# Kernel optimization log

Hardware: AMD Instinct MI355X
Metric: run time of the kernel (lower is better)

## Reference

```python
import jax, jax.numpy as jnp
import numpy as np

HEAD_NUM = 4
B, S, D = 8, 1024, 512


def setup_inputs() -> dict:
    k = jax.random.key(0)
    kq, kk, kv = jax.random.split(k, 3)
    return {
        "query": jax.random.normal(kq, (B, S, D), dtype=jnp.float32),
        "key": jax.random.normal(kk, (B, S, D), dtype=jnp.float32),
        "value": jax.random.normal(kv, (B, S, D), dtype=jnp.float32),
    }


def _corr_attention(q, k, v):
    # q,k,v: [B, H, S, hd]
    score = jnp.einsum('bhqd,bhkd->bhqk', q, k)  # raw dot products
    len_q = jnp.sqrt(jnp.sum(q * q, axis=-1))    # [B,H,S]
    len_k = jnp.sqrt(jnp.sum(k * k, axis=-1))    # [B,H,S]
    score = score / (len_q[..., :, None] * len_k[..., None, :])  # cosine similarity
    signal = jnp.sign(score)
    flat = jnp.abs(score).reshape(-1)            # global flatten across B,H,S,S
    n = flat.shape[0]
    idx = jnp.argsort(-flat)                     # descending sort indices
    prob = (jnp.arange(n, dtype=flat.dtype) + 1.0) / n  # (1/n, 2/n, ..., 1)
    ranked = flat.at[idx].set(prob)              # rank-transform: largest -> smallest prob
    score = (-jnp.log(ranked)).reshape(signal.shape) * signal
    return jnp.einsum('bhqk,bhkd->bhqd', score, v)


def reference(query, key, value):
    b, s, d = query.shape
    h = HEAD_NUM
    q = query.reshape(b, s, h, -1).transpose(0, 2, 1, 3)
    k = key.reshape(b, s, h, -1).transpose(0, 2, 1, 3)
    v = value.reshape(b, s, h, -1).transpose(0, 2, 1, 3)
    out = _corr_attention(q, k, v)               # [B,H,S,hd]
    return out.transpose(0, 2, 1, 3).reshape(b, s, d)
```

## Files before the change

kernel.cpp:

```cpp
#include <hip/hip_runtime.h>
#include <math.h>

#define BB 8
#define SS 1024
#define DD 512
#define HH 4
#define HD 128
#define N_SC (BB*HH*SS*SS)

#define NB 8192
#define BINA 20971.52f
#define NPART 512

#define OFF_S     0
#define SZ_S      ((size_t)N_SC*2)
#define OFF_QN    (OFF_S + SZ_S)
#define SZ_QN     ((size_t)BB*SS*DD*2)
#define OFF_KN    (OFF_QN + SZ_QN)
#define OFF_VT    (OFF_KN + SZ_QN)
#define OFF_PARTS (OFF_VT + SZ_QN)
#define SZ_PARTS  ((size_t)NPART*NB*2)
#define OFF_HIST  (OFF_PARTS + SZ_PARTS)

typedef __bf16 bf16x8 __attribute__((ext_vector_type(8)));
typedef float  f32x4  __attribute__((ext_vector_type(4)));
typedef unsigned short ushort_t;

__device__ __forceinline__ unsigned bf16rne(float x) {
  unsigned b = __float_as_uint(x);
  return (b + 0x7FFFu + ((b >> 16) & 1u)) >> 16;
}

__global__ __launch_bounds__(256) void prep_kernel(
    const float* __restrict__ q, const float* __restrict__ k,
    unsigned* __restrict__ qn, unsigned* __restrict__ kn) {
  int t = threadIdx.x, lane = t & 63;
  int row = blockIdx.x*4 + (t >> 6);
  const float* src; unsigned* dst; int r;
  if (row < 32768) { src = q; dst = qn; r = row; }
  else             { src = k; dst = kn; r = row - 32768; }
  int b = r >> 12, s = (r >> 2) & 1023, h = r & 3;
  float2 v = *(const float2*)(src + ((size_t)(b*1024 + s))*512 + h*128 + lane*2);
  float sum = v.x*v.x + v.y*v.y;
  #pragma unroll
  for (int off = 32; off; off >>= 1) sum += __shfl_xor(sum, off, 64);
  float inv = rsqrtf(sum);
  unsigned u = bf16rne(v.x*inv) | (bf16rne(v.y*inv) << 16);
  dst[(size_t)((b*4 + h)*1024 + s)*64 + lane] = u;
}

__global__ __launch_bounds__(256) void vt_kernel(
    const float* __restrict__ v, unsigned* __restrict__ vt) {
  __shared__ float T[64][65];
  int t = threadIdx.x;
  int s0 = blockIdx.x*64, d0 = blockIdx.y*64, bh = blockIdx.z;
  int b = bh >> 2, h = bh & 3;
  #pragma unroll
  for (int i = 0; i < 16; i++) {
    int idx = t + i*256, rs = idx >> 6, cd = idx & 63;
    T[rs][cd] = v[((size_t)(b*1024 + s0 + rs))*512 + h*128 + d0 + cd];
  }
  __syncthreads();
  #pragma unroll
  for (int i = 0; i < 8; i++) {
    int idx = t + i*256, rd = idx >> 5, c2 = (idx & 31)*2;
    unsigned u = bf16rne(T[c2][rd]) | (bf16rne(T[c2+1][rd]) << 16);
    vt[(size_t)(bh*128 + d0 + rd)*512 + (s0 + c2)/2] = u;
  }
}

__global__ __launch_bounds__(256) void scores_kernel(
    const ushort_t* __restrict__ qn, const ushort_t* __restrict__ kn,
    ushort_t* __restrict__ S) {
  __shared__ ushort_t Qs[128*128];
  __shared__ ushort_t Ks[128*128];
  int t = threadIdx.x;
  int bh = blockIdx.z, sq0 = blockIdx.y*128, sk0 = blockIdx.x*128;

  const uint4* qg = (const uint4*)qn + (size_t)(bh*1024 + sq0)*16;
  const uint4* kg = (const uint4*)kn + (size_t)(bh*1024 + sk0)*16;
  #pragma unroll
  for (int i = 0; i < 8; i++) {
    int idx = t + i*256, row = idx >> 4, g = idx & 15;
    int sw = g ^ (row & 15);
    *(uint4*)&Qs[row*128 + sw*8] = qg[row*16 + g];
    *(uint4*)&Ks[row*128 + sw*8] = kg[row*16 + g];
  }
  __syncthreads();

  int w = t >> 6, lane = t & 63, m16 = lane & 15, q2 = lane >> 4;
  int wm = (w >> 1)*64, wn = (w & 1)*64;
  f32x4 acc[4][4];
  #pragma unroll
  for (int i = 0; i < 4; i++)
    #pragma unroll
    for (int j = 0; j < 4; j++) acc[i][j] = (f32x4){0.f,0.f,0.f,0.f};

  #pragma unroll
  for (int ks = 0; ks < 4; ks++) {
    int sw = ((ks*4 + q2) ^ m16)*8;
    bf16x8 a[4], bb[4];
    #pragma unroll
    for (int i = 0; i < 4; i++) a[i]  = *(const bf16x8*)&Qs[(wm + i*16 + m16)*128 + sw];
    #pragma unroll
    for (int j = 0; j < 4; j++) bb[j] = *(const bf16x8*)&Ks[(wn + j*16 + m16)*128 + sw];
    #pragma unroll
    for (int i = 0; i < 4; i++)
      #pragma unroll
      for (int j = 0; j < 4; j++)
        acc[i][j] = __builtin_amdgcn_mfma_f32_16x16x32_bf16(a[i], bb[j], acc[i][j], 0, 0, 0);
  }

  size_t Sbase = (size_t)bh << 20;
  #pragma unroll
  for (int i = 0; i < 4; i++)
    #pragma unroll
    for (int p = 0; p < 4; p++) {
      int row = sq0 + wm + i*16 + q2*4 + p;
      #pragma unroll
      for (int j = 0; j < 4; j++) {
        int col = sk0 + wn + j*16 + m16;
        S[Sbase + ((size_t)row << 10) + col] = (ushort_t)bf16rne(acc[i][j][p]);
      }
    }
}

__global__ __launch_bounds__(1024) void hist_kernel(
    const ushort_t* __restrict__ S, ushort_t* __restrict__ parts) {
  __shared__ unsigned h[NB];
  int t = threadIdx.x;
  #pragma unroll
  for (int i = t; i < NB; i += 1024) h[i] = 0;
  __syncthreads();
  const uint4* p = (const uint4*)S;
  size_t base = (size_t)blockIdx.x * 8192;
  #pragma unroll
  for (int it = 0; it < 8; it++) {
    uint4 v = p[base + t + it*1024];
    unsigned ws[4] = {v.x, v.y, v.z, v.w};
    #pragma unroll
    for (int j = 0; j < 4; j++) {
      float flo = __uint_as_float(ws[j] << 16);
      float fhi = __uint_as_float(ws[j] & 0xFFFF0000u);
      atomicAdd(&h[(unsigned)fminf(flo*flo*BINA, 8191.0f)], 1u);
      atomicAdd(&h[(unsigned)fminf(fhi*fhi*BINA, 8191.0f)], 1u);
    }
  }
  __syncthreads();
  ushort_t* dst = parts + (size_t)blockIdx.x*NB;
  for (int i = t; i < NB; i += 1024) dst[i] = (ushort_t)min(h[i], 65535u);
}

__global__ __launch_bounds__(256) void reduce_kernel(
    const ushort_t* __restrict__ parts, unsigned* __restrict__ hist) {
  int bin = blockIdx.x*256 + threadIdx.x;
  unsigned s = 0;
  #pragma unroll 8
  for (int p = 0; p < NPART; p++) s += parts[(size_t)p*NB + bin];
  hist[bin] = s;
}

__global__ __launch_bounds__(1024) void scan_kernel(unsigned* hist) {
  __shared__ unsigned d[1024];
  int t = threadIdx.x;
  unsigned loc[8];
  uint4 a = ((const uint4*)hist)[t*2], b2 = ((const uint4*)hist)[t*2+1];
  loc[0]=a.x; loc[1]=a.y; loc[2]=a.z; loc[3]=a.w;
  loc[4]=b2.x; loc[5]=b2.y; loc[6]=b2.z; loc[7]=b2.w;
  unsigned tot = 0;
  #pragma unroll
  for (int j = 0; j < 8; j++) tot += loc[j];
  d[t] = tot; __syncthreads();
  for (int off = 1; off < 1024; off <<= 1) {
    unsigned x = (t >= off) ? d[t - off] : 0u;
    __syncthreads();
    d[t] += x;
    __syncthreads();
  }
  unsigned run = d[t] - tot;
  const float inv_n = 1.0f / (float)N_SC;
  float* w = (float*)hist;
  #pragma unroll
  for (int j = 0; j < 8; j++) {
    run += loc[j];
    float rm = (float)(N_SC - run) + 0.5f*(float)(loc[j] + 1u);
    w[t*8 + j] = -logf(rm * inv_n);
  }
}

__global__ __launch_bounds__(256) void out_kernel(
    const ushort_t* __restrict__ S, const float* __restrict__ wmag,
    const ushort_t* __restrict__ vt, float* __restrict__ out) {
  __shared__ ushort_t Ws[64*128];
  __shared__ ushort_t Vs[128*128];
  __shared__ float    Wl[NB];
  int t = threadIdx.x;
  int bh = blockIdx.y, q0 = blockIdx.x*64;
  int b = bh >> 2, h = bh & 3;

  #pragma unroll
  for (int i = 0; i < 8; i++) {
    int idx = t + i*256;
    ((uint4*)Wl)[idx] = ((const uint4*)wmag)[idx];
  }

  int w = t >> 6, lane = t & 63, m16 = lane & 15, q2 = lane >> 4;
  int wq = (w >> 1)*32, wd = (w & 1)*64;
  f32x4 acc[2][4];
  #pragma unroll
  for (int i = 0; i < 2; i++)
    #pragma unroll
    for (int j = 0; j < 4; j++) acc[i][j] = (f32x4){0.f,0.f,0.f,0.f};

  for (int kc = 0; kc < 8; kc++) {
    __syncthreads();
    #pragma unroll
    for (int i = 0; i < 4; i++) {
      int idx = t + i*256, row = idx >> 4, g = idx & 15;
      uint4 sv = ((const uint4*)S)[(size_t)(bh*1024 + q0 + row)*128 + kc*16 + g];
      unsigned wsrc[4] = {sv.x, sv.y, sv.z, sv.w};
      unsigned wdst[4];
      #pragma unroll
      for (int j = 0; j < 4; j++) {
        float flo = __uint_as_float(wsrc[j] << 16);
        float fhi = __uint_as_float(wsrc[j] & 0xFFFF0000u);
        float mlo = Wl[(unsigned)fminf(flo*flo*BINA, 8191.0f)];
        float mhi = Wl[(unsigned)fminf(fhi*fhi*BINA, 8191.0f)];
        float wlo = (flo == 0.f) ? 0.f : copysignf(mlo, flo);
        float whi = (fhi == 0.f) ? 0.f : copysignf(mhi, fhi);
        wdst[j] = bf16rne(wlo) | (bf16rne(whi) << 16);
      }
      uint4 wv = {wdst[0], wdst[1], wdst[2], wdst[3]};
      *(uint4*)&Ws[row*128 + ((g ^ (row & 15))*8)] = wv;
    }
    #pragma unroll
    for (int i = 0; i < 8; i++) {
      int idx = t + i*256, row = idx >> 4, g = idx & 15;
      uint4 vv = ((const uint4*)vt)[(size_t)(bh*128 + row)*128 + kc*16 + g];
      *(uint4*)&Vs[row*128 + ((g ^ (row & 15))*8)] = vv;
    }
    __syncthreads();
    #pragma unroll
    for (int ks = 0; ks < 4; ks++) {
      int sw = ((ks*4 + q2) ^ m16)*8;
      bf16x8 a[2], bb[4];
      #pragma unroll
      for (int i = 0; i < 2; i++) a[i]  = *(const bf16x8*)&Ws[(wq + i*16 + m16)*128 + sw];
      #pragma unroll
      for (int j = 0; j < 4; j++) bb[j] = *(const bf16x8*)&Vs[(wd + j*16 + m16)*128 + sw];
      #pragma unroll
      for (int i = 0; i < 2; i++)
        #pragma unroll
        for (int j = 0; j < 4; j++)
          acc[i][j] = __builtin_amdgcn_mfma_f32_16x16x32_bf16(a[i], bb[j], acc[i][j], 0, 0, 0);
    }
  }

  #pragma unroll
  for (int i = 0; i < 2; i++)
    #pragma unroll
    for (int p = 0; p < 4; p++) {
      int qrow = q0 + wq + i*16 + q2*4 + p;
      #pragma unroll
      for (int j = 0; j < 4; j++) {
        int dcol = wd + j*16 + m16;
        out[(size_t)(b*1024 + qrow)*512 + h*128 + dcol] = acc[i][j][p];
      }
    }
}

extern "C" void kernel_launch(void* const* d_in, const int* in_sizes, int n_in,
                              void* d_out, int out_size, void* d_ws, size_t ws_size,
                              hipStream_t stream) {
  const float* q = (const float*)d_in[0];
  const float* k = (const float*)d_in[1];
  const float* v = (const float*)d_in[2];
  float* out = (float*)d_out;
  char* ws = (char*)d_ws;

  ushort_t* Sbuf  = (ushort_t*)(ws + OFF_S);
  unsigned* qn    = (unsigned*)(ws + OFF_QN);
  unsigned* kn    = (unsigned*)(ws + OFF_KN);
  unsigned* vtb   = (unsigned*)(ws + OFF_VT);
  ushort_t* parts = (ushort_t*)(ws + OFF_PARTS);
  unsigned* hist  = (unsigned*)(ws + OFF_HIST);

  hipLaunchKernelGGL(prep_kernel, dim3(16384), dim3(256), 0, stream, q, k, qn, kn);
  hipLaunchKernelGGL(vt_kernel, dim3(16, 2, 32), dim3(256), 0, stream, v, vtb);
  hipLaunchKernelGGL(scores_kernel, dim3(8, 8, 32), dim3(256), 0, stream,
                     (const ushort_t*)qn, (const ushort_t*)kn, Sbuf);
  hipLaunchKernelGGL(hist_kernel, dim3(NPART), dim3(1024), 0, stream, Sbuf, parts);
  hipLaunchKernelGGL(reduce_kernel, dim3(NB/256), dim3(256), 0, stream, parts, hist);
  hipLaunchKernelGGL(scan_kernel, dim3(1), dim3(1024), 0, stream, hist);
  hipLaunchKernelGGL(out_kernel, dim3(16, 32), dim3(256), 0, stream,
                     Sbuf, (const float*)hist, (const ushort_t*)vtb, out);
}
```

Before: 186.2 us.

## Fuse histogram into score GEMM and recompute scores in output kernel

The full bf16 score matrix is no longer written to global memory. The score kernel now builds a per-block histogram in shared memory, packing four 8-bit counters per word, and writes only the partial histograms. The output kernel recomputes Q·K^T per tile and maps each score to its rank weight through an LDS lookup table before the PV MFMA. The prep and V-transpose kernels are merged into one launch, the weight table is stored as bf16, and binning is switched from squared to linear magnitude. This removes a large write and two large reads of the score matrix, at the cost of a second QK GEMM. An 8-bit bin overflows if more than 255 scores in one block land in the same bin, and V is now read straight from global memory in the inner loop.

```diff
diff --git a/kernel.cpp b/kernel.cpp
--- a/kernel.cpp
+++ b/kernel.cpp
@@ -9,18 +9,17 @@
 #define N_SC (BB*HH*SS*SS)
 
 #define NB 8192
-#define BINA 20971.52f
-#define NPART 512
-
-#define OFF_S     0
-#define SZ_S      ((size_t)N_SC*2)
-#define OFF_QN    (OFF_S + SZ_S)
+#define BINS 13107.2f
+#define NBLK 2048
+
+#define OFF_QN    0
 #define SZ_QN     ((size_t)BB*SS*DD*2)
 #define OFF_KN    (OFF_QN + SZ_QN)
 #define OFF_VT    (OFF_KN + SZ_QN)
 #define OFF_PARTS (OFF_VT + SZ_QN)
-#define SZ_PARTS  ((size_t)NPART*NB*2)
+#define SZ_PARTS  ((size_t)NBLK*(NB/4)*4)
 #define OFF_HIST  (OFF_PARTS + SZ_PARTS)
+#define OFF_WMAG  (OFF_HIST + (size_t)NB*4)
 
 typedef __bf16 bf16x8 __attribute__((ext_vector_type(8)));
 typedef float  f32x4  __attribute__((ext_vector_type(4)));
@@ -30,52 +29,61 @@
   unsigned b = __float_as_uint(x);
   return (b + 0x7FFFu + ((b >> 16) & 1u)) >> 16;
 }
-
-__global__ __launch_bounds__(256) void prep_kernel(
+__device__ __forceinline__ unsigned sbin(float s) {
+  return (unsigned)fminf(fabsf(s)*BINS, 8191.0f);
+}
+
+__global__ __launch_bounds__(256) void prep_vt_kernel(
     const float* __restrict__ q, const float* __restrict__ k,
-    unsigned* __restrict__ qn, unsigned* __restrict__ kn) {
-  int t = threadIdx.x, lane = t & 63;
-  int row = blockIdx.x*4 + (t >> 6);
-  const float* src; unsigned* dst; int r;
-  if (row < 32768) { src = q; dst = qn; r = row; }
-  else             { src = k; dst = kn; r = row - 32768; }
-  int b = r >> 12, s = (r >> 2) & 1023, h = r & 3;
-  float2 v = *(const float2*)(src + ((size_t)(b*1024 + s))*512 + h*128 + lane*2);
-  float sum = v.x*v.x + v.y*v.y;
-  #pragma unroll
-  for (int off = 32; off; off >>= 1) sum += __shfl_xor(sum, off, 64);
-  float inv = rsqrtf(sum);
-  unsigned u = bf16rne(v.x*inv) | (bf16rne(v.y*inv) << 16);
-  dst[(size_t)((b*4 + h)*1024 + s)*64 + lane] = u;
-}
-
-__global__ __launch_bounds__(256) void vt_kernel(
-    const float* __restrict__ v, unsigned* __restrict__ vt) {
+    const float* __restrict__ v,
+    unsigned* __restrict__ qn, unsigned* __restrict__ kn,
+    unsigned* __restrict__ vt) {
   __shared__ float T[64][65];
   int t = threadIdx.x;
-  int s0 = blockIdx.x*64, d0 = blockIdx.y*64, bh = blockIdx.z;
-  int b = bh >> 2, h = bh & 3;
-  #pragma unroll
-  for (int i = 0; i < 16; i++) {
-    int idx = t + i*256, rs = idx >> 6, cd = idx & 63;
-    T[rs][cd] = v[((size_t)(b*1024 + s0 + rs))*512 + h*128 + d0 + cd];
-  }
-  __syncthreads();
-  #pragma unroll
-  for (int i = 0; i < 8; i++) {
-    int idx = t + i*256, rd = idx >> 5, c2 = (idx & 31)*2;
-    unsigned u = bf16rne(T[c2][rd]) | (bf16rne(T[c2+1][rd]) << 16);
-    vt[(size_t)(bh*128 + d0 + rd)*512 + (s0 + c2)/2] = u;
-  }
-}
-
-__global__ __launch_bounds__(256) void scores_kernel(
+  if (blockIdx.x < 16384) {
+    int lane = t & 63;
+    int row = blockIdx.x*4 + (t >> 6);
+    const float* src; unsigned* dst; int r;
+    if (row < 32768) { src = q; dst = qn; r = row; }
+    else             { src = k; dst = kn; r = row - 32768; }
+    int b = r >> 12, s = (r >> 2) & 1023, h = r & 3;
+    float2 vv = *(const float2*)(src + ((size_t)(b*1024 + s))*512 + h*128 + lane*2);
+    float sum = vv.x*vv.x + vv.y*vv.y;
+    #pragma unroll
+    for (int off = 32; off; off >>= 1) sum += __shfl_xor(sum, off, 64);
+    float inv = rsqrtf(sum);
+    unsigned u = bf16rne(vv.x*inv) | (bf16rne(vv.y*inv) << 16);
+    dst[(size_t)((b*4 + h)*1024 + s)*64 + lane] = u;
+  } else {
+    int vb = blockIdx.x - 16384;
+    int s0 = (vb & 15)*64, d0 = ((vb >> 4) & 1)*64, bh = vb >> 5;
+    int b = bh >> 2, h = bh & 3;
+    #pragma unroll
+    for (int i = 0; i < 16; i++) {
+      int idx = t + i*256, rs = idx >> 6, cd = idx & 63;
+      T[rs][cd] = v[((size_t)(b*1024 + s0 + rs))*512 + h*128 + d0 + cd];
+    }
+    __syncthreads();
+    #pragma unroll
+    for (int i = 0; i < 8; i++) {
+      int idx = t + i*256, rd = idx >> 5, c2 = (idx & 31)*2;
+      unsigned u = bf16rne(T[c2][rd]) | (bf16rne(T[c2+1][rd]) << 16);
+      vt[(size_t)(bh*128 + d0 + rd)*512 + (s0 + c2)/2] = u;
+    }
+  }
+}
+
+__global__ __launch_bounds__(256) void scores_hist_kernel(
     const ushort_t* __restrict__ qn, const ushort_t* __restrict__ kn,
-    ushort_t* __restrict__ S) {
+    unsigned* __restrict__ parts) {
   __shared__ ushort_t Qs[128*128];
   __shared__ ushort_t Ks[128*128];
+  __shared__ unsigned h8[NB/4];
   int t = threadIdx.x;
   int bh = blockIdx.z, sq0 = blockIdx.y*128, sk0 = blockIdx.x*128;
+
+  #pragma unroll
+  for (int i = 0; i < 8; i++) h8[t + i*256] = 0;
 
   const uint4* qg = (const uint4*)qn + (size_t)(bh*1024 + sq0)*16;
   const uint4* kg = (const uint4*)kn + (size_t)(bh*1024 + sk0)*16;
@@ -111,56 +119,39 @@
         acc[i][j] = __builtin_amdgcn_mfma_f32_16x16x32_bf16(a[i], bb[j], acc[i][j], 0, 0, 0);
   }
 
-  size_t Sbase = (size_t)bh << 20;
   #pragma unroll
   for (int i = 0; i < 4; i++)
     #pragma unroll
-    for (int p = 0; p < 4; p++) {
-      int row = sq0 + wm + i*16 + q2*4 + p;
-      #pragma unroll
-      for (int j = 0; j < 4; j++) {
-        int col = sk0 + wn + j*16 + m16;
-        S[Sbase + ((size_t)row << 10) + col] = (ushort_t)bf16rne(acc[i][j][p]);
+    for (int j = 0; j < 4; j++)
+      #pragma unroll
+      for (int p = 0; p < 4; p++) {
+        unsigned bin = sbin(acc[i][j][p]);
+        atomicAdd(&h8[bin >> 2], 1u << ((bin & 3)*8));
       }
-    }
-}
-
-__global__ __launch_bounds__(1024) void hist_kernel(
-    const ushort_t* __restrict__ S, ushort_t* __restrict__ parts) {
-  __shared__ unsigned h[NB];
-  int t = threadIdx.x;
-  #pragma unroll
-  for (int i = t; i < NB; i += 1024) h[i] = 0;
   __syncthreads();
-  const uint4* p = (const uint4*)S;
-  size_t base = (size_t)blockIdx.x * 8192;
-  #pragma unroll
-  for (int it = 0; it < 8; it++) {
-    uint4 v = p[base + t + it*1024];
-    unsigned ws[4] = {v.x, v.y, v.z, v.w};
-    #pragma unroll
-    for (int j = 0; j < 4; j++) {
-      float flo = __uint_as_float(ws[j] << 16);
-      float fhi = __uint_as_float(ws[j] & 0xFFFF0000u);
-      atomicAdd(&h[(unsigned)fminf(flo*flo*BINA, 8191.0f)], 1u);
-      atomicAdd(&h[(unsigned)fminf(fhi*fhi*BINA, 8191.0f)], 1u);
-    }
-  }
-  __syncthreads();
-  ushort_t* dst = parts + (size_t)blockIdx.x*NB;
-  for (int i = t; i < NB; i += 1024) dst[i] = (ushort_t)min(h[i], 65535u);
+
+  int blockId = (bh*64) + blockIdx.y*8 + blockIdx.x;
+  unsigned* dst = parts + (size_t)blockId*(NB/4);
+  #pragma unroll
+  for (int i = 0; i < 8; i++) dst[t + i*256] = h8[t + i*256];
 }
 
 __global__ __launch_bounds__(256) void reduce_kernel(
-    const ushort_t* __restrict__ parts, unsigned* __restrict__ hist) {
-  int bin = blockIdx.x*256 + threadIdx.x;
-  unsigned s = 0;
+    const unsigned* __restrict__ parts, unsigned* __restrict__ hist) {
+  int g = blockIdx.x*256 + threadIdx.x;
+  unsigned s0 = 0, s1 = 0, s2 = 0, s3 = 0;
   #pragma unroll 8
-  for (int p = 0; p < NPART; p++) s += parts[(size_t)p*NB + bin];
-  hist[bin] = s;
-}
-
-__global__ __launch_bounds__(1024) void scan_kernel(unsigned* hist) {
+  for (int p = 0; p < NBLK; p++) {
+    unsigned w = parts[(size_t)p*(NB/4) + g];
+    s0 += w & 0xFFu; s1 += (w >> 8) & 0xFFu;
+    s2 += (w >> 16) & 0xFFu; s3 += w >> 24;
+  }
+  uint4 o = {s0, s1, s2, s3};
+  ((uint4*)hist)[g] = o;
+}
+
+__global__ __launch_bounds__(1024) void scan_kernel(
+    const unsigned* __restrict__ hist, ushort_t* __restrict__ wmag) {
   __shared__ unsigned d[1024];
   int t = threadIdx.x;
   unsigned loc[8];
@@ -179,80 +170,105 @@
   }
   unsigned run = d[t] - tot;
   const float inv_n = 1.0f / (float)N_SC;
-  float* w = (float*)hist;
   #pragma unroll
   for (int j = 0; j < 8; j++) {
     run += loc[j];
     float rm = (float)(N_SC - run) + 0.5f*(float)(loc[j] + 1u);
-    w[t*8 + j] = -logf(rm * inv_n);
+    wmag[t*8 + j] = (ushort_t)bf16rne(-logf(rm * inv_n));
   }
 }
 
 __global__ __launch_bounds__(256) void out_kernel(
-    const ushort_t* __restrict__ S, const float* __restrict__ wmag,
-    const ushort_t* __restrict__ vt, float* __restrict__ out) {
+    const ushort_t* __restrict__ qn, const ushort_t* __restrict__ kn,
+    const ushort_t* __restrict__ wmag, const ushort_t* __restrict__ vt,
+    float* __restrict__ out) {
+  __shared__ ushort_t Qs[64*128];
+  __shared__ ushort_t Ks[128*128];
   __shared__ ushort_t Ws[64*128];
-  __shared__ ushort_t Vs[128*128];
-  __shared__ float    Wl[NB];
+  __shared__ ushort_t Wl[NB];
   int t = threadIdx.x;
   int bh = blockIdx.y, q0 = blockIdx.x*64;
   int b = bh >> 2, h = bh & 3;
 
   #pragma unroll
-  for (int i = 0; i < 8; i++) {
-    int idx = t + i*256;
-    ((uint4*)Wl)[idx] = ((const uint4*)wmag)[idx];
+  for (int i = 0; i < 4; i++)
+    ((uint4*)Wl)[t + i*256] = ((const uint4*)wmag)[t + i*256];
+
+  const uint4* qg = (const uint4*)qn + (size_t)(bh*1024 + q0)*16;
+  #pragma unroll
+  for (int i = 0; i < 4; i++) {
+    int idx = t + i*256, row = idx >> 4, g = idx & 15;
+    *(uint4*)&Qs[row*128 + (g ^ (row & 15))*8] = qg[row*16 + g];
   }
 
   int w = t >> 6, lane = t & 63, m16 = lane & 15, q2 = lane >> 4;
   int wq = (w >> 1)*32, wd = (w & 1)*64;
-  f32x4 acc[2][4];
+  f32x4 oacc[2][4];
   #pragma unroll
   for (int i = 0; i < 2; i++)
     #pragma unroll
-    for (int j = 0; j < 4; j++) acc[i][j] = (f32x4){0.f,0.f,0.f,0.f};
+    for (int j = 0; j < 4; j++) oacc[i][j] = (f32x4){0.f,0.f,0.f,0.f};
 
   for (int kc = 0; kc < 8; kc++) {
-    __syncthreads();
-    #pragma unroll
-    for (int i = 0; i < 4; i++) {
-      int idx = t + i*256, row = idx >> 4, g = idx & 15;
-      uint4 sv = ((const uint4*)S)[(size_t)(bh*1024 + q0 + row)*128 + kc*16 + g];
-      unsigned wsrc[4] = {sv.x, sv.y, sv.z, sv.w};
-      unsigned wdst[4];
-      #pragma unroll
-      for (int j = 0; j < 4; j++) {
-        float flo = __uint_as_float(wsrc[j] << 16);
-        float fhi = __uint_as_float(wsrc[j] & 0xFFFF0000u);
-        float mlo = Wl[(unsigned)fminf(flo*flo*BINA, 8191.0f)];
-        float mhi = Wl[(unsigned)fminf(fhi*fhi*BINA, 8191.0f)];
-        float wlo = (flo == 0.f) ? 0.f : copysignf(mlo, flo);
-        float whi = (fhi == 0.f) ? 0.f : copysignf(mhi, fhi);
-        wdst[j] = bf16rne(wlo) | (bf16rne(whi) << 16);
-      }
-      uint4 wv = {wdst[0], wdst[1], wdst[2], wdst[3]};
-      *(uint4*)&Ws[row*128 + ((g ^ (row & 15))*8)] = wv;
-    }
+    const uint4* kg = (const uint4*)kn + (size_t)(bh*1024 + kc*128)*16;
     #pragma unroll
     for (int i = 0; i < 8; i++) {
       int idx = t + i*256, row = idx >> 4, g = idx & 15;
-      uint4 vv = ((const uint4*)vt)[(size_t)(bh*128 + row)*128 + kc*16 + g];
-      *(uint4*)&Vs[row*128 + ((g ^ (row & 15))*8)] = vv;
-    }
-    __syncthreads();
+      *(uint4*)&Ks[row*128 + (g ^ (row & 15))*8] = kg[row*16 + g];
+    }
+    __syncthreads();
+
+    f32x4 sacc[2][4];
+    #pragma unroll
+    for (int i = 0; i < 2; i++)
+      #pragma unroll
+      for (int j = 0; j < 4; j++) sacc[i][j] = (f32x4){0.f,0.f,0.f,0.f};
     #pragma unroll
     for (int ks = 0; ks < 4; ks++) {
       int sw = ((ks*4 + q2) ^ m16)*8;
       bf16x8 a[2], bb[4];
       #pragma unroll
-      for (int i = 0; i < 2; i++) a[i]  = *(const bf16x8*)&Ws[(wq + i*16 + m16)*128 + sw];
-      #pragma unroll
-      for (int j = 0; j < 4; j++) bb[j] = *(const bf16x8*)&Vs[(wd + j*16 + m16)*128 + sw];
+      for (int i = 0; i < 2; i++) a[i]  = *(const bf16x8*)&Qs[(wq + i*16 + m16)*128 + sw];
+      #pragma unroll
+      for (int j = 0; j < 4; j++) bb[j] = *(const bf16x8*)&Ks[(wd + j*16 + m16)*128 + sw];
       #pragma unroll
       for (int i = 0; i < 2; i++)
         #pragma unroll
         for (int j = 0; j < 4; j++)
-          acc[i][j] = __builtin_amdgcn_mfma_f32_16x16x32_bf16(a[i], bb[j], acc[i][j], 0, 0, 0);
+          sacc[i][j] = __builtin_amdgcn_mfma_f32_16x16x32_bf16(a[i], bb[j], sacc[i][j], 0, 0, 0);
+    }
+    __syncthreads();
+
+    #pragma unroll
+    for (int i = 0; i < 2; i++)
+      #pragma unroll
+      for (int j = 0; j < 4; j++)
+        #pragma unroll
+        for (int p = 0; p < 4; p++) {
+          float s = sacc[i][j][p];
+          unsigned wm = (s == 0.f) ? 0u
+                        : (unsigned)Wl[sbin(s)] | ((s < 0.f) ? 0x8000u : 0u);
+          int row = wq + i*16 + q2*4 + p;
+          int col = wd + j*16 + m16;
+          Ws[row*128 + ((col >> 3) ^ (row & 15))*8 + (col & 7)] = (ushort_t)wm;
+        }
+    __syncthreads();
+
+    const uint4* vg = (const uint4*)vt;
+    #pragma unroll
+    for (int ks = 0; ks < 4; ks++) {
+      int sw = ((ks*4 + q2) ^ m16)*8;
+      bf16x8 a[2], bb[4];
+      #pragma unroll
+      for (int i = 0; i < 2; i++) a[i] = *(const bf16x8*)&Ws[(wq + i*16 + m16)*128 + sw];
+      #pragma unroll
+      for (int j = 0; j < 4; j++)
+        bb[j] = *(const bf16x8*)&vg[(size_t)(bh*128 + wd + j*16 + m16)*128 + kc*16 + ks*4 + q2];
+      #pragma unroll
+      for (int i = 0; i < 2; i++)
+        #pragma unroll
+        for (int j = 0; j < 4; j++)
+          oacc[i][j] = __builtin_amdgcn_mfma_f32_16x16x32_bf16(a[i], bb[j], oacc[i][j], 0, 0, 0);
     }
   }
 
@@ -264,7 +280,7 @@
       #pragma unroll
       for (int j = 0; j < 4; j++) {
         int dcol = wd + j*16 + m16;
-        out[(size_t)(b*1024 + qrow)*512 + h*128 + dcol] = acc[i][j][p];
+        out[(size_t)(b*1024 + qrow)*512 + h*128 + dcol] = oacc[i][j][p];
       }
     }
 }
@@ -278,20 +294,19 @@
   float* out = (float*)d_out;
   char* ws = (char*)d_ws;
 
-  ushort_t* Sbuf  = (ushort_t*)(ws + OFF_S);
   unsigned* qn    = (unsigned*)(ws + OFF_QN);
   unsigned* kn    = (unsigned*)(ws + OFF_KN);
   unsigned* vtb   = (unsigned*)(ws + OFF_VT);
-  ushort_t* parts = (ushort_t*)(ws + OFF_PARTS);
+  unsigned* parts = (unsigned*)(ws + OFF_PARTS);
   unsigned* hist  = (unsigned*)(ws + OFF_HIST);
-
-  hipLaunchKernelGGL(prep_kernel, dim3(16384), dim3(256), 0, stream, q, k, qn, kn);
-  hipLaunchKernelGGL(vt_kernel, dim3(16, 2, 32), dim3(256), 0, stream, v, vtb);
-  hipLaunchKernelGGL(scores_kernel, dim3(8, 8, 32), dim3(256), 0, stream,
-                     (const ushort_t*)qn, (const ushort_t*)kn, Sbuf);
-  hipLaunchKernelGGL(hist_kernel, dim3(NPART), dim3(1024), 0, stream, Sbuf, parts);
-  hipLaunchKernelGGL(reduce_kernel, dim3(NB/256), dim3(256), 0, stream, parts, hist);
-  hipLaunchKernelGGL(scan_kernel, dim3(1), dim3(1024), 0, stream, hist);
+  ushort_t* wmag  = (ushort_t*)(ws + OFF_WMAG);
+
+  hipLaunchKernelGGL(prep_vt_kernel, dim3(17408), dim3(256), 0, stream, q, k, v, qn, kn, vtb);
+  hipLaunchKernelGGL(scores_hist_kernel, dim3(8, 8, 32), dim3(256), 0, stream,
+                     (const ushort_t*)qn, (const ushort_t*)kn, parts);
+  hipLaunchKernelGGL(reduce_kernel, dim3(8), dim3(256), 0, stream, parts, hist);
+  hipLaunchKernelGGL(scan_kernel, dim3(1), dim3(1024), 0, stream, hist, wmag);
   hipLaunchKernelGGL(out_kernel, dim3(16, 32), dim3(256), 0, stream,
-                     Sbuf, (const float*)hist, (const ushort_t*)vtb, out);
-}
+                     (const ushort_t*)qn, (const ushort_t*)kn, wmag,
+                     (const ushort_t*)vtb, out);
+}
```

After: 253.9 us. +36.3%, slower.
